# Optimization experiments

Measured on AMD Instinct MI355X. Metric: run time of the kernel, lower is better.

## Reference

```python
import jax, jax.numpy as jnp
import numpy as np

N_NODES = 50000


def _spmm(edge_index, edge_vals, dense):
    """Sparse [N,N] @ dense [N,D] via gather + segment-sum.
    edge_index[0] = row (dst), edge_index[1] = col (src)."""
    dst, src = edge_index[0], edge_index[1]
    msgs = edge_vals[:, None] * dense[src]  # [E, D]
    return jax.ops.segment_sum(msgs, dst, num_segments=N_NODES)


def setup_inputs() -> dict:
    key = jax.random.key(0)
    ks = jax.random.split(key, 8)
    N, D_IN, D_OUT, E = N_NODES, 128, 128, 800000
    x = jax.random.normal(ks[0], (N, D_IN), dtype=jnp.float32)
    # glorot init for weights
    scale = jnp.sqrt(6.0 / (D_IN + D_OUT)).astype(jnp.float32)
    W0 = jax.random.uniform(ks[1], (D_IN, D_OUT), jnp.float32, -scale, scale)
    W1 = jax.random.uniform(ks[2], (D_IN, D_OUT), jnp.float32, -scale, scale)
    bias = jnp.zeros((D_OUT,), dtype=jnp.float32)
    edge_vals0 = jax.random.uniform(ks[3], (E,), dtype=jnp.float32)
    edge_vals1 = jax.random.uniform(ks[4], (E,), dtype=jnp.float32)
    edge_index0 = jax.random.randint(ks[5], (2, E), 0, N, dtype=jnp.int32)
    edge_index1 = jax.random.randint(ks[6], (2, E), 0, N, dtype=jnp.int32)
    return {"x": x, "W0": W0, "W1": W1, "bias": bias,
            "edge_vals0": edge_vals0, "edge_vals1": edge_vals1,
            "edge_index0": edge_index0, "edge_index1": edge_index1}


def reference(x, W0, W1, bias, edge_vals0, edge_vals1, edge_index0, edge_index1):
    # dropout with rate 0 == identity (self.dropout unset in source snippet)
    pre0 = x @ W0  # [N, D_out]
    pre1 = x @ W1
    out = _spmm(edge_index0, edge_vals0, pre0) + _spmm(edge_index1, edge_vals1, pre1)
    out = out + bias
    return jax.nn.relu(out)
```

## Files before the change

### kernel.cpp

```cpp
#include <hip/hip_runtime.h>
#include <hip/hip_bf16.h>


#define BROWS 32
#define NBUCK 1563
#define BCAP 704
#define ACAP (2 * BCAP)
#define FT 16384

typedef __attribute__((ext_vector_type(8))) short bf16x8;
typedef __attribute__((ext_vector_type(4))) float f32x4;

__device__ inline unsigned short f2bf(float f) {
    union { float f; unsigned u; } v; v.f = f;
    unsigned r = v.u + 0x7fff + ((v.u >> 16) & 1);
    return (unsigned short)(r >> 16);
}

__global__ __launch_bounds__(256) void convert_w_kernel(
    const float* __restrict__ W0, const float* __restrict__ W1,
    unsigned short* __restrict__ wt0, unsigned short* __restrict__ wt1)
{
    const float* __restrict__ W = blockIdx.x ? W1 : W0;
    unsigned short* __restrict__ wt = blockIdx.x ? wt1 : wt0;
    for (int i = threadIdx.x; i < 128 * 128; i += 256) {
        int k = i >> 7, n = i & 127;
        wt[n * 128 + k] = f2bf(W[i]);
    }
}

__global__ __launch_bounds__(512) void gemm_fused_kernel(
    const float* __restrict__ x,
    const unsigned short* __restrict__ wt0,
    const unsigned short* __restrict__ wt1,
    unsigned short* __restrict__ pre0,
    unsigned short* __restrict__ pre1, int N)
{
    const int w = threadIdx.x >> 6;
    const int lane = threadIdx.x & 63;
    const int adj = w >> 2;
    const int wq = w & 3;
    const int m0 = blockIdx.x * 16;
    const unsigned short* __restrict__ wt = adj ? wt1 : wt0;
    unsigned short* __restrict__ pre = adj ? pre1 : pre0;
    const int l15 = lane & 15;
    const int quad = lane >> 4;
    const int nA = wq * 32 + l15;

    f32x4 c0 = {0.f, 0.f, 0.f, 0.f};
    f32x4 c1 = {0.f, 0.f, 0.f, 0.f};
#pragma unroll
    for (int k0 = 0; k0 < 128; k0 += 32) {
        const float* xp = &x[(m0 + l15) * 128 + k0 + quad * 8];
        float4 v0 = *(const float4*)xp;
        float4 v1 = *(const float4*)(xp + 4);
        bf16x8 a;
        ((short*)&a)[0] = (short)f2bf(v0.x);
        ((short*)&a)[1] = (short)f2bf(v0.y);
        ((short*)&a)[2] = (short)f2bf(v0.z);
        ((short*)&a)[3] = (short)f2bf(v0.w);
        ((short*)&a)[4] = (short)f2bf(v1.x);
        ((short*)&a)[5] = (short)f2bf(v1.y);
        ((short*)&a)[6] = (short)f2bf(v1.z);
        ((short*)&a)[7] = (short)f2bf(v1.w);
        bf16x8 b0 = *(const bf16x8*)&wt[nA * 128 + k0 + quad * 8];
        bf16x8 b1 = *(const bf16x8*)&wt[(nA + 16) * 128 + k0 + quad * 8];
        c0 = __builtin_amdgcn_mfma_f32_16x16x32_bf16(a, b0, c0, 0, 0, 0);
        c1 = __builtin_amdgcn_mfma_f32_16x16x32_bf16(a, b1, c1, 0, 0, 0);
    }
#pragma unroll
    for (int i = 0; i < 4; ++i) {
        int row = m0 + quad * 4 + i;
        pre[row * 128 + wq * 32 + l15] = f2bf(c0[i]);
        pre[row * 128 + wq * 32 + 16 + l15] = f2bf(c1[i]);
    }
}

__global__ __launch_bounds__(1024) void fill4_kernel(
    const int* __restrict__ ei0, const int* __restrict__ ei1,
    const float* __restrict__ ev0, const float* __restrict__ ev1,
    int* __restrict__ cur, int2* __restrict__ recs, int E)
{
    const int a = blockIdx.y;
    const int* __restrict__ ei = a ? ei1 : ei0;
    const float* __restrict__ ev = a ? ev1 : ev0;

    __shared__ int lcnt[NBUCK];
    __shared__ int gbase[NBUCK];
    __shared__ int glim[NBUCK];
    for (int k = threadIdx.x; k < NBUCK; k += 1024) lcnt[k] = 0;
    __syncthreads();

    const int e0 = blockIdx.x * FT;
    unsigned ds[16];
    float val[16];
    short rank[16];
#pragma unroll
    for (int j = 0; j < 16; ++j) {
        int e = e0 + j * 1024 + threadIdx.x;
        if (e < E) {
            int d = ei[e];
            int s = ei[E + e];
            ds[j] = ((unsigned)d << 16) | (unsigned)s;
            val[j] = ev[e];
            rank[j] = (short)atomicAdd(&lcnt[d >> 5], 1);
        } else ds[j] = 0xffffffffu;
    }
    __syncthreads();

    for (int k = threadIdx.x; k < NBUCK; k += 1024) {
        int c = lcnt[k];
        int base = 0, lim = 0;
        if (c > 0) {
            int bin = k * 2 + a;
            int b0 = atomicAdd(&cur[bin], c);
            lim = BCAP - b0; if (lim < 0) lim = 0;
            base = bin * BCAP + b0;
        }
        gbase[k] = base;
        glim[k] = lim;
    }
    __syncthreads();

#pragma unroll
    for (int j = 0; j < 16; ++j) {
        if (ds[j] != 0xffffffffu) {
            int key = ds[j] >> 21;
            int r = rank[j];
            if (r < glim[key]) {
                int rl = (ds[j] >> 16) & 31;
                recs[gbase[key] + r] =
                    make_int2((rl << 16) | (ds[j] & 0xffff), __float_as_int(val[j]));
            }
        }
    }
}

__global__ __launch_bounds__(256) void aggregate8_kernel(
    const int* __restrict__ cur, const int2* __restrict__ recs,
    const unsigned short* __restrict__ pre0,
    const unsigned short* __restrict__ pre1,
    const float* __restrict__ bias,
    float* __restrict__ out, int N)
{
    __shared__ int2 srec[ACAP];
    __shared__ unsigned short sidx[ACAP];
    __shared__ int lcnt[64];
    __shared__ int lstart[64];
    __shared__ int lcur[64];

    const int b = blockIdx.x;
    const int tid = threadIdx.x;

    int n0 = cur[2 * b];     if (n0 > BCAP) n0 = BCAP;
    int n1 = cur[2 * b + 1]; if (n1 > BCAP) n1 = BCAP;
    const int total = n0 + n1;
    const int base0 = (2 * b) * BCAP, base1 = (2 * b + 1) * BCAP;

    if (tid < 64) lcnt[tid] = 0;
    __syncthreads();

    for (int i = tid; i < total; i += 256) {
        int2 r = (i < n0) ? recs[base0 + i] : recs[base1 + i - n0];
        srec[i] = r;
        int a = (i >= n0);
        atomicAdd(&lcnt[(a << 5) | (r.x >> 16)], 1);
    }
    __syncthreads();

    if (tid < 64) {
        int cme = lcnt[tid];
        int p = cme;
#pragma unroll
        for (int o = 1; o < 64; o <<= 1) {
            int t = __shfl_up(p, o);
            if (tid >= o) p += t;
        }
        lstart[tid] = p - cme;
        lcur[tid] = p - cme;
    }
    __syncthreads();

    for (int i = tid; i < total; i += 256) {
        int a = (i >= n0);
        int key = (a << 5) | (srec[i].x >> 16);
        sidx[atomicAdd(&lcur[key], 1)] = (unsigned short)i;
    }
    __syncthreads();

    const int wv = tid >> 6;
    const int lane = tid & 63;
    const float2 bi = *(const float2*)&bias[lane * 2];

    for (int t = 0; t < 8; ++t) {
        const int rl = wv * 8 + t;
        float2 acc = make_float2(0.f, 0.f);
#pragma unroll
        for (int a = 0; a < 2; ++a) {
            const unsigned short* __restrict__ pre = a ? pre1 : pre0;
            const int key = (a << 5) | rl;
            const int s = lstart[key];
            const int n = lcnt[key];
            int j = 0;
            for (; j + 4 <= n; j += 4) {
                int i0 = sidx[s + j + 0];
                int i1 = sidx[s + j + 1];
                int i2 = sidx[s + j + 2];
                int i3 = sidx[s + j + 3];
                int2 r0 = srec[i0], r1 = srec[i1], r2 = srec[i2], r3 = srec[i3];
                unsigned u0 = *(const unsigned*)&pre[(r0.x & 0xffff) * 128 + 2 * lane];
                unsigned u1 = *(const unsigned*)&pre[(r1.x & 0xffff) * 128 + 2 * lane];
                unsigned u2 = *(const unsigned*)&pre[(r2.x & 0xffff) * 128 + 2 * lane];
                unsigned u3 = *(const unsigned*)&pre[(r3.x & 0xffff) * 128 + 2 * lane];
                float v0 = __int_as_float(r0.y), v1 = __int_as_float(r1.y);
                float v2 = __int_as_float(r2.y), v3 = __int_as_float(r3.y);
                acc.x = fmaf(v0, __uint_as_float(u0 << 16), acc.x);
                acc.y = fmaf(v0, __uint_as_float(u0 & 0xffff0000u), acc.y);
                acc.x = fmaf(v1, __uint_as_float(u1 << 16), acc.x);
                acc.y = fmaf(v1, __uint_as_float(u1 & 0xffff0000u), acc.y);
                acc.x = fmaf(v2, __uint_as_float(u2 << 16), acc.x);
                acc.y = fmaf(v2, __uint_as_float(u2 & 0xffff0000u), acc.y);
                acc.x = fmaf(v3, __uint_as_float(u3 << 16), acc.x);
                acc.y = fmaf(v3, __uint_as_float(u3 & 0xffff0000u), acc.y);
            }
            for (; j < n; ++j) {
                int2 r0 = srec[sidx[s + j]];
                unsigned u0 = *(const unsigned*)&pre[(r0.x & 0xffff) * 128 + 2 * lane];
                float v0 = __int_as_float(r0.y);
                acc.x = fmaf(v0, __uint_as_float(u0 << 16), acc.x);
                acc.y = fmaf(v0, __uint_as_float(u0 & 0xffff0000u), acc.y);
            }
        }
        int row = b * BROWS + rl;
        if (row < N) {
            float2 o;
            o.x = fmaxf(acc.x + bi.x, 0.f);
            o.y = fmaxf(acc.y + bi.y, 0.f);
            *(float2*)&out[row * 128 + 2 * lane] = o;
        }
    }
}

extern "C" void kernel_launch(void* const* d_in, const int* in_sizes, int n_in,
                              void* d_out, int out_size, void* d_ws, size_t ws_size,
                              hipStream_t stream) {
    const float* x    = (const float*)d_in[0];
    const float* W0   = (const float*)d_in[1];
    const float* W1   = (const float*)d_in[2];
    const float* bias = (const float*)d_in[3];
    const float* ev0  = (const float*)d_in[4];
    const float* ev1  = (const float*)d_in[5];
    const int*   ei0  = (const int*)d_in[6];
    const int*   ei1  = (const int*)d_in[7];
    float* out = (float*)d_out;

    const int N = in_sizes[0] / 128;
    const int E = in_sizes[4];
    const int NX = N * 128;
    const int NBINS2 = NBUCK * 2;

    char* w = (char*)d_ws;
    unsigned short* pre0 = (unsigned short*)w;  w += (size_t)NX * 2;
    unsigned short* pre1 = (unsigned short*)w;  w += (size_t)NX * 2;
    unsigned short* wt0  = (unsigned short*)w;  w += (size_t)128 * 128 * 2;
    unsigned short* wt1  = (unsigned short*)w;  w += (size_t)128 * 128 * 2;
    int* cur = (int*)w;                         w += (size_t)NBINS2 * 4;
    int2* recs = (int2*)w;                      w += (size_t)NBINS2 * BCAP * 8;

    convert_w_kernel<<<2, 256, 0, stream>>>(W0, W1, wt0, wt1);

    gemm_fused_kernel<<<N / 16, 512, 0, stream>>>(x, wt0, wt1, pre0, pre1, N);

    hipMemsetAsync(cur, 0, (size_t)NBINS2 * 4, stream);
    dim3 fgrid((E + FT - 1) / FT, 2);
    fill4_kernel<<<fgrid, 1024, 0, stream>>>(ei0, ei1, ev0, ev1, cur, recs, E);

    aggregate8_kernel<<<NBUCK, 256, 0, stream>>>(cur, recs, pre0, pre1,
                                                 bias, out, N);
}
```

Before: 250.0 us.

## Merge pre buffers, sort records directly, fold memset, shrink fill tile, vectorize GEMM stores

Several changes land together. The two pre buffers are merged into one array indexed by a 17-bit row that carries the adjacency bit, so aggregation sorts full records by destination row instead of an index array and runs a single 8-way unrolled gather loop. The cur memset moves into extra blocks of the weight-convert kernel, and the fill tile shrinks to 4096 so more blocks run in parallel. GEMM outputs are staged through LDS so each lane writes 16-byte vector stores, and the aggregation kernel gets an occupancy hint. The costs are more global atomics in fill from the extra blocks, added LDS use in the GEMM, and register pressure from the hint.

```diff
diff --git a/kernel.cpp b/kernel.cpp
--- a/kernel.cpp
+++ b/kernel.cpp
@@ -6,7 +6,8 @@
 #define NBUCK 1563
 #define BCAP 704
 #define ACAP (2 * BCAP)
-#define FT 16384
+#define FT 4096
+#define PREROWS 65536
 
 typedef __attribute__((ext_vector_type(8))) short bf16x8;
 typedef __attribute__((ext_vector_type(4))) float f32x4;
@@ -19,8 +20,16 @@
 
 __global__ __launch_bounds__(256) void convert_w_kernel(
     const float* __restrict__ W0, const float* __restrict__ W1,
-    unsigned short* __restrict__ wt0, unsigned short* __restrict__ wt1)
-{
+    unsigned short* __restrict__ wt0, unsigned short* __restrict__ wt1,
+    int* __restrict__ cur, int ncur)
+{
+    if (blockIdx.x >= 2) {
+        int half = (ncur + 1) / 2;
+        int base = (blockIdx.x - 2) * half;
+        for (int i = threadIdx.x; i < half; i += 256)
+            if (base + i < ncur) cur[base + i] = 0;
+        return;
+    }
     const float* __restrict__ W = blockIdx.x ? W1 : W0;
     unsigned short* __restrict__ wt = blockIdx.x ? wt1 : wt0;
     for (int i = threadIdx.x; i < 128 * 128; i += 256) {
@@ -33,16 +42,18 @@
     const float* __restrict__ x,
     const unsigned short* __restrict__ wt0,
     const unsigned short* __restrict__ wt1,
-    unsigned short* __restrict__ pre0,
-    unsigned short* __restrict__ pre1, int N)
-{
+    unsigned short* __restrict__ pre,
+    int N)
+{
+    __shared__ short ctile[8][16][40];
+
     const int w = threadIdx.x >> 6;
     const int lane = threadIdx.x & 63;
     const int adj = w >> 2;
     const int wq = w & 3;
     const int m0 = blockIdx.x * 16;
     const unsigned short* __restrict__ wt = adj ? wt1 : wt0;
-    unsigned short* __restrict__ pre = adj ? pre1 : pre0;
+    unsigned short* __restrict__ po = pre + (size_t)adj * PREROWS * 128;
     const int l15 = lane & 15;
     const int quad = lane >> 4;
     const int nA = wq * 32 + l15;
@@ -68,12 +79,18 @@
         c0 = __builtin_amdgcn_mfma_f32_16x16x32_bf16(a, b0, c0, 0, 0, 0);
         c1 = __builtin_amdgcn_mfma_f32_16x16x32_bf16(a, b1, c1, 0, 0, 0);
     }
+
 #pragma unroll
     for (int i = 0; i < 4; ++i) {
-        int row = m0 + quad * 4 + i;
-        pre[row * 128 + wq * 32 + l15] = f2bf(c0[i]);
-        pre[row * 128 + wq * 32 + 16 + l15] = f2bf(c1[i]);
-    }
+        ctile[w][quad * 4 + i][l15]      = (short)f2bf(c0[i]);
+        ctile[w][quad * 4 + i][16 + l15] = (short)f2bf(c1[i]);
+    }
+    const int rr = lane >> 2, cg = (lane & 3) * 8;
+    ushort4 s0 = *(ushort4*)&ctile[w][rr][cg];
+    ushort4 s1 = *(ushort4*)&ctile[w][rr][cg + 4];
+    int row = m0 + rr;
+    *(ushort4*)&po[row * 128 + wq * 32 + cg] = s0;
+    *(ushort4*)&po[row * 128 + wq * 32 + cg + 4] = s1;
 }
 
 __global__ __launch_bounds__(1024) void fill4_kernel(
@@ -92,11 +109,11 @@
     __syncthreads();
 
     const int e0 = blockIdx.x * FT;
-    unsigned ds[16];
-    float val[16];
-    short rank[16];
-#pragma unroll
-    for (int j = 0; j < 16; ++j) {
+    unsigned ds[4];
+    float val[4];
+    short rank[4];
+#pragma unroll
+    for (int j = 0; j < 4; ++j) {
         int e = e0 + j * 1024 + threadIdx.x;
         if (e < E) {
             int d = ei[e];
@@ -123,31 +140,31 @@
     __syncthreads();
 
 #pragma unroll
-    for (int j = 0; j < 16; ++j) {
+    for (int j = 0; j < 4; ++j) {
         if (ds[j] != 0xffffffffu) {
             int key = ds[j] >> 21;
             int r = rank[j];
             if (r < glim[key]) {
                 int rl = (ds[j] >> 16) & 31;
                 recs[gbase[key] + r] =
-                    make_int2((rl << 16) | (ds[j] & 0xffff), __float_as_int(val[j]));
+                    make_int2((rl << 17) | (a << 16) | (ds[j] & 0xffff),
+                              __float_as_int(val[j]));
             }
         }
     }
 }
 
-__global__ __launch_bounds__(256) void aggregate8_kernel(
+__global__ __launch_bounds__(256, 6) void aggregate9_kernel(
     const int* __restrict__ cur, const int2* __restrict__ recs,
-    const unsigned short* __restrict__ pre0,
-    const unsigned short* __restrict__ pre1,
+    const unsigned short* __restrict__ pre,
     const float* __restrict__ bias,
     float* __restrict__ out, int N)
 {
     __shared__ int2 srec[ACAP];
-    __shared__ unsigned short sidx[ACAP];
-    __shared__ int lcnt[64];
-    __shared__ int lstart[64];
-    __shared__ int lcur[64];
+    __shared__ int2 srt[ACAP];
+    __shared__ int lcnt[32];
+    __shared__ int lstart[32];
+    __shared__ int lcur[32];
 
     const int b = blockIdx.x;
     const int tid = threadIdx.x;
@@ -157,22 +174,21 @@
     const int total = n0 + n1;
     const int base0 = (2 * b) * BCAP, base1 = (2 * b + 1) * BCAP;
 
-    if (tid < 64) lcnt[tid] = 0;
+    if (tid < 32) lcnt[tid] = 0;
     __syncthreads();
 
     for (int i = tid; i < total; i += 256) {
         int2 r = (i < n0) ? recs[base0 + i] : recs[base1 + i - n0];
         srec[i] = r;
-        int a = (i >= n0);
-        atomicAdd(&lcnt[(a << 5) | (r.x >> 16)], 1);
-    }
-    __syncthreads();
-
-    if (tid < 64) {
+        atomicAdd(&lcnt[(r.x >> 17) & 31], 1);
+    }
+    __syncthreads();
+
+    if (tid < 32) {
         int cme = lcnt[tid];
         int p = cme;
 #pragma unroll
-        for (int o = 1; o < 64; o <<= 1) {
+        for (int o = 1; o < 32; o <<= 1) {
             int t = __shfl_up(p, o);
             if (tid >= o) p += t;
         }
@@ -182,9 +198,8 @@
     __syncthreads();
 
     for (int i = tid; i < total; i += 256) {
-        int a = (i >= n0);
-        int key = (a << 5) | (srec[i].x >> 16);
-        sidx[atomicAdd(&lcur[key], 1)] = (unsigned short)i;
+        int2 r = srec[i];
+        srt[atomicAdd(&lcur[(r.x >> 17) & 31], 1)] = r;
     }
     __syncthreads();
 
@@ -192,44 +207,34 @@
     const int lane = tid & 63;
     const float2 bi = *(const float2*)&bias[lane * 2];
 
+#define GA(r) (*(const unsigned*)&pre[((r).x & 0x1ffff) * 128 + 2 * lane])
+#define ACC(r, u) { float v = __int_as_float((r).y);                    \
+        acc.x = fmaf(v, __uint_as_float((u) << 16), acc.x);             \
+        acc.y = fmaf(v, __uint_as_float((u) & 0xffff0000u), acc.y); }
+
     for (int t = 0; t < 8; ++t) {
         const int rl = wv * 8 + t;
+        const int s = lstart[rl];
+        const int e = s + lcnt[rl];
         float2 acc = make_float2(0.f, 0.f);
-#pragma unroll
-        for (int a = 0; a < 2; ++a) {
-            const unsigned short* __restrict__ pre = a ? pre1 : pre0;
-            const int key = (a << 5) | rl;
-            const int s = lstart[key];
-            const int n = lcnt[key];
-            int j = 0;
-            for (; j + 4 <= n; j += 4) {
-                int i0 = sidx[s + j + 0];
-                int i1 = sidx[s + j + 1];
-                int i2 = sidx[s + j + 2];
-                int i3 = sidx[s + j + 3];
-                int2 r0 = srec[i0], r1 = srec[i1], r2 = srec[i2], r3 = srec[i3];
-                unsigned u0 = *(const unsigned*)&pre[(r0.x & 0xffff) * 128 + 2 * lane];
-                unsigned u1 = *(const unsigned*)&pre[(r1.x & 0xffff) * 128 + 2 * lane];
-                unsigned u2 = *(const unsigned*)&pre[(r2.x & 0xffff) * 128 + 2 * lane];
-                unsigned u3 = *(const unsigned*)&pre[(r3.x & 0xffff) * 128 + 2 * lane];
-                float v0 = __int_as_float(r0.y), v1 = __int_as_float(r1.y);
-                float v2 = __int_as_float(r2.y), v3 = __int_as_float(r3.y);
-                acc.x = fmaf(v0, __uint_as_float(u0 << 16), acc.x);
-                acc.y = fmaf(v0, __uint_as_float(u0 & 0xffff0000u), acc.y);
-                acc.x = fmaf(v1, __uint_as_float(u1 << 16), acc.x);
-                acc.y = fmaf(v1, __uint_as_float(u1 & 0xffff0000u), acc.y);
-                acc.x = fmaf(v2, __uint_as_float(u2 << 16), acc.x);
-                acc.y = fmaf(v2, __uint_as_float(u2 & 0xffff0000u), acc.y);
-                acc.x = fmaf(v3, __uint_as_float(u3 << 16), acc.x);
-                acc.y = fmaf(v3, __uint_as_float(u3 & 0xffff0000u), acc.y);
-            }
-            for (; j < n; ++j) {
-                int2 r0 = srec[sidx[s + j]];
-                unsigned u0 = *(const unsigned*)&pre[(r0.x & 0xffff) * 128 + 2 * lane];
-                float v0 = __int_as_float(r0.y);
-                acc.x = fmaf(v0, __uint_as_float(u0 << 16), acc.x);
-                acc.y = fmaf(v0, __uint_as_float(u0 & 0xffff0000u), acc.y);
-            }
+        int j = s;
+        for (; j + 8 <= e; j += 8) {
+            int2 r0 = srt[j], r1 = srt[j + 1], r2 = srt[j + 2], r3 = srt[j + 3];
+            int2 r4 = srt[j + 4], r5 = srt[j + 5], r6 = srt[j + 6], r7 = srt[j + 7];
+            unsigned u0 = GA(r0), u1 = GA(r1), u2 = GA(r2), u3 = GA(r3);
+            unsigned u4 = GA(r4), u5 = GA(r5), u6 = GA(r6), u7 = GA(r7);
+            ACC(r0, u0); ACC(r1, u1); ACC(r2, u2); ACC(r3, u3);
+            ACC(r4, u4); ACC(r5, u5); ACC(r6, u6); ACC(r7, u7);
+        }
+        for (; j + 4 <= e; j += 4) {
+            int2 r0 = srt[j], r1 = srt[j + 1], r2 = srt[j + 2], r3 = srt[j + 3];
+            unsigned u0 = GA(r0), u1 = GA(r1), u2 = GA(r2), u3 = GA(r3);
+            ACC(r0, u0); ACC(r1, u1); ACC(r2, u2); ACC(r3, u3);
+        }
+        for (; j < e; ++j) {
+            int2 r0 = srt[j];
+            unsigned u0 = GA(r0);
+            ACC(r0, u0);
         }
         int row = b * BROWS + rl;
         if (row < N) {
@@ -239,6 +244,8 @@
             *(float2*)&out[row * 128 + 2 * lane] = o;
         }
     }
+#undef GA
+#undef ACC
 }
 
 extern "C" void kernel_launch(void* const* d_in, const int* in_sizes, int n_in,
@@ -256,25 +263,21 @@
 
     const int N = in_sizes[0] / 128;
     const int E = in_sizes[4];
-    const int NX = N * 128;
     const int NBINS2 = NBUCK * 2;
 
     char* w = (char*)d_ws;
-    unsigned short* pre0 = (unsigned short*)w;  w += (size_t)NX * 2;
-    unsigned short* pre1 = (unsigned short*)w;  w += (size_t)NX * 2;
-    unsigned short* wt0  = (unsigned short*)w;  w += (size_t)128 * 128 * 2;
-    unsigned short* wt1  = (unsigned short*)w;  w += (size_t)128 * 128 * 2;
+    unsigned short* pre = (unsigned short*)w;   w += (size_t)2 * PREROWS * 128 * 2;
+    unsigned short* wt0 = (unsigned short*)w;   w += (size_t)128 * 128 * 2;
+    unsigned short* wt1 = (unsigned short*)w;   w += (size_t)128 * 128 * 2;
     int* cur = (int*)w;                         w += (size_t)NBINS2 * 4;
     int2* recs = (int2*)w;                      w += (size_t)NBINS2 * BCAP * 8;
 
-    convert_w_kernel<<<2, 256, 0, stream>>>(W0, W1, wt0, wt1);
-
-    gemm_fused_kernel<<<N / 16, 512, 0, stream>>>(x, wt0, wt1, pre0, pre1, N);
-
-    hipMemsetAsync(cur, 0, (size_t)NBINS2 * 4, stream);
+    convert_w_kernel<<<4, 256, 0, stream>>>(W0, W1, wt0, wt1, cur, NBINS2);
+
+    gemm_fused_kernel<<<N / 16, 512, 0, stream>>>(x, wt0, wt1, pre, N);
+
     dim3 fgrid((E + FT - 1) / FT, 2);
     fill4_kernel<<<fgrid, 1024, 0, stream>>>(ei0, ei1, ev0, ev1, cur, recs, E);
 
-    aggregate8_kernel<<<NBUCK, 256, 0, stream>>>(cur, recs, pre0, pre1,
-                                                 bias, out, N);
-}
+    aggregate9_kernel<<<NBUCK, 256, 0, stream>>>(cur, recs, pre, bias, out, N);
+}
```

New measurement: 239.0 us. 1.05x faster.
